# Kernel optimization log

Hardware: AMD Instinct MI355X
Metric: run time of the kernel (lower is better)

The kernel has to match this reference:

```python
import jax, jax.numpy as jnp
import numpy as np

B, S, T = 4, 1024, 2048
HID = 1024
NH = 16
NKV = 4
HD = HID // NH  # 64


def setup_inputs() -> dict:
    key = jax.random.key(0)
    ks = jax.random.split(key, 6)
    scale = 1.0 / np.sqrt(HID)
    return {
        "x": jax.random.normal(ks[0], (B, S, HID), dtype=jnp.float32),
        "context": jax.random.normal(ks[1], (B, T, HID), dtype=jnp.float32),
        "Wq": jax.random.normal(ks[2], (NH * HD, HID), dtype=jnp.float32) * scale,
        "Wk": jax.random.normal(ks[3], (NKV * HD, HID), dtype=jnp.float32) * scale,
        "Wv": jax.random.normal(ks[4], (NKV * HD, HID), dtype=jnp.float32) * scale,
        "Wo": jax.random.normal(ks[5], (HID, NH * HD), dtype=jnp.float32) * scale,
    }


def reference(x, context, Wq, Wk, Wv, Wo):
    Bx, Sx, _ = x.shape
    Tx = context.shape[1]
    rep = NH // NKV
    # projections (Linear with no bias: y = x @ W.T)
    q = (x @ Wq.T).reshape(Bx, Sx, NKV, rep, HD)          # group query heads by KV head
    k = (context @ Wk.T).reshape(Bx, Tx, NKV, HD)
    v = (context @ Wv.T).reshape(Bx, Tx, NKV, HD)
    scale = 1.0 / jnp.sqrt(jnp.asarray(HD, dtype=q.dtype))
    # scores: [B, NKV, rep, S, T] -- shares K across the rep grouped heads
    # (math-identical to repeat_interleave then SDPA, without materializing K/V copies)
    scores = jnp.einsum("bsgrd,btgd->bgrst", q, k) * scale
    attn = jax.nn.softmax(scores, axis=-1)
    out = jnp.einsum("bgrst,btgd->bsgrd", attn, v)        # [B,S,NKV,rep,HD]
    out = out.reshape(Bx, Sx, NH * HD)
    return out @ Wo.T
```

## Files before the change

kernel.cpp:

```cpp
#include <hip/hip_runtime.h>
#include <hip/hip_bf16.h>
#include <stdint.h>

typedef __bf16 bf16x8 __attribute__((ext_vector_type(8)));
typedef float f32x4 __attribute__((ext_vector_type(4)));
typedef unsigned short u16;
typedef unsigned int u32;

struct __align__(8) us4 { u16 x, y, z, w; };
struct __align__(16) us8 { u16 v[8]; };

#define LOG2E 1.44269504088896f
#define QSCALE (0.125f * LOG2E)

__device__ __forceinline__ void async_load16(const void* g, void* l) {
    __builtin_amdgcn_global_load_lds(
        (const __attribute__((address_space(1))) u32*)(uintptr_t)g,
        (__attribute__((address_space(3))) u32*)(u32)(uintptr_t)l,
        16, 0, 0);
}

__device__ __forceinline__ u16 f2bfbits(float f) {
    __bf16 h = (__bf16)f;
    return __builtin_bit_cast(u16, h);
}

__global__ __launch_bounds__(256) void convert_all(
    const float* __restrict__ x, const float* __restrict__ ctx,
    const float* __restrict__ wq, const float* __restrict__ wk,
    const float* __restrict__ wv, const float* __restrict__ wo,
    u16* __restrict__ xb, u16* __restrict__ ctxb, u16* __restrict__ wqb,
    u16* __restrict__ wkb, u16* __restrict__ wvb, u16* __restrict__ wob) {
    int i = blockIdx.x * 256 + threadIdx.x;
    const float* s; u16* d; int j;
    if (i < 524288)        { s = x;   d = xb;   j = i; }
    else if (i < 1572864)  { s = ctx; d = ctxb; j = i - 524288; }
    else if (i < 1703936)  { s = wq;  d = wqb;  j = i - 1572864; }
    else if (i < 1736704)  { s = wk;  d = wkb;  j = i - 1703936; }
    else if (i < 1769472)  { s = wv;  d = wvb;  j = i - 1736704; }
    else                   { s = wo;  d = wob;  j = i - 1769472; }
    const float4* sp = (const float4*)s + (size_t)j * 2;
    float4 a = sp[0], b = sp[1];
    us8 o;
    o.v[0] = f2bfbits(a.x); o.v[1] = f2bfbits(a.y);
    o.v[2] = f2bfbits(a.z); o.v[3] = f2bfbits(a.w);
    o.v[4] = f2bfbits(b.x); o.v[5] = f2bfbits(b.y);
    o.v[6] = f2bfbits(b.z); o.v[7] = f2bfbits(b.w);
    *(us8*)(d + (size_t)j * 8) = o;
}

__global__ __launch_bounds__(256) void proj_qkv(
    const u16* __restrict__ xb, const u16* __restrict__ ctxb,
    const u16* __restrict__ Wqb, const u16* __restrict__ Wkb,
    const u16* __restrict__ Wvb,
    u16* __restrict__ q, u16* __restrict__ k2, u16* __restrict__ vT) {
    __shared__ u16 As[128 * 64];
    __shared__ u16 Bs[128 * 64];
    const int tid = threadIdx.x;
    const int w = tid >> 6, lane = tid & 63, quad = lane >> 4, id = lane & 15;
    const int wr = (w >> 1) * 64, wc = (w & 1) * 64;
    const int lrow = lane >> 3, lcol = (lane & 7) * 8;

    const int bid = blockIdx.x;
    const u16 *A, *Bm;
    int mtile, ntile, mode;
    if (bid < 256) {
        mode = 0; A = xb; Bm = Wqb;
        mtile = (bid >> 3) * 128; ntile = (bid & 7) * 128;
    } else {
        int t = bid - 256, z = t >> 7, r = t & 127;
        mode = 1 + z; A = ctxb; Bm = z ? Wvb : Wkb;
        mtile = (r >> 1) * 128; ntile = (r & 1) * 128;
    }

    f32x4 acc[4][4];
#pragma unroll
    for (int i = 0; i < 4; i++)
#pragma unroll
        for (int j = 0; j < 4; j++) acc[i][j] = (f32x4){0.f, 0.f, 0.f, 0.f};

    for (int k0 = 0; k0 < 1024; k0 += 64) {
        __syncthreads();
#pragma unroll
        for (int is = 0; is < 4; is++) {
            int r = is * 32 + w * 8 + lrow;
            async_load16(A + (size_t)(mtile + r) * 1024 + k0 + lcol, &As[(is * 32 + w * 8) * 64]);
        }
#pragma unroll
        for (int is = 0; is < 4; is++) {
            int r = is * 32 + w * 8 + lrow;
            async_load16(Bm + (size_t)(ntile + r) * 1024 + k0 + lcol, &Bs[(is * 32 + w * 8) * 64]);
        }
        __syncthreads();
#pragma unroll
        for (int kk = 0; kk < 2; kk++) {
            bf16x8 af[4], bfr[4];
#pragma unroll
            for (int i = 0; i < 4; i++)
                af[i] = *(const bf16x8*)&As[(wr + i * 16 + id) * 64 + kk * 32 + quad * 8];
#pragma unroll
            for (int j = 0; j < 4; j++)
                bfr[j] = *(const bf16x8*)&Bs[(wc + j * 16 + id) * 64 + kk * 32 + quad * 8];
#pragma unroll
            for (int i = 0; i < 4; i++)
#pragma unroll
                for (int j = 0; j < 4; j++)
                    acc[i][j] = __builtin_amdgcn_mfma_f32_16x16x32_bf16(af[i], bfr[j], acc[i][j], 0, 0, 0);
        }
    }

#pragma unroll
    for (int i = 0; i < 4; i++)
#pragma unroll
        for (int j = 0; j < 4; j++) {
            int mbase = mtile + wr + i * 16 + quad * 4;
            int n = ntile + wc + j * 16 + id;
            if (mode == 2) {
                int b = mbase >> 11, t = mbase & 2047;
                int g = n >> 6, d = n & 63;
                us4 pk;
                pk.x = f2bfbits(acc[i][j][0]);
                pk.y = f2bfbits(acc[i][j][1]);
                pk.z = f2bfbits(acc[i][j][2]);
                pk.w = f2bfbits(acc[i][j][3]);
                *(us4*)&vT[((size_t)((b << 2) + g) * 64 + d) * 2048 + t] = pk;
            } else if (mode == 1) {
#pragma unroll
                for (int r = 0; r < 4; r++) {
                    int m = mbase + r;
                    int b = m >> 11, t = m & 2047;
                    int g = n >> 6, d = n & 63;
                    k2[((size_t)((b << 2) + g) * 2048 + t) * 64 + d] = f2bfbits(acc[i][j][r]);
                }
            } else {
#pragma unroll
                for (int r = 0; r < 4; r++)
                    q[(size_t)(mbase + r) * 1024 + n] = f2bfbits(acc[i][j][r] * QSCALE);
            }
        }
}

__global__ __launch_bounds__(256) void gemm_out(const u16* __restrict__ A,
                                                const u16* __restrict__ Bm,
                                                float* __restrict__ C) {
    __shared__ u16 As[128 * 64];
    __shared__ u16 Bs[128 * 64];
    const int tid = threadIdx.x;
    const int w = tid >> 6, lane = tid & 63, quad = lane >> 4, id = lane & 15;
    const int mtile = blockIdx.y * 128, ntile = blockIdx.x * 128;
    const int wr = (w >> 1) * 64, wc = (w & 1) * 64;
    const int lrow = lane >> 3, lcol = (lane & 7) * 8;

    f32x4 acc[4][4];
#pragma unroll
    for (int i = 0; i < 4; i++)
#pragma unroll
        for (int j = 0; j < 4; j++) acc[i][j] = (f32x4){0.f, 0.f, 0.f, 0.f};

    for (int k0 = 0; k0 < 1024; k0 += 64) {
        __syncthreads();
#pragma unroll
        for (int is = 0; is < 4; is++) {
            int r = is * 32 + w * 8 + lrow;
            async_load16(A + (size_t)(mtile + r) * 1024 + k0 + lcol, &As[(is * 32 + w * 8) * 64]);
        }
#pragma unroll
        for (int is = 0; is < 4; is++) {
            int r = is * 32 + w * 8 + lrow;
            async_load16(Bm + (size_t)(ntile + r) * 1024 + k0 + lcol, &Bs[(is * 32 + w * 8) * 64]);
        }
        __syncthreads();
#pragma unroll
        for (int kk = 0; kk < 2; kk++) {
            bf16x8 af[4], bfr[4];
#pragma unroll
            for (int i = 0; i < 4; i++)
                af[i] = *(const bf16x8*)&As[(wr + i * 16 + id) * 64 + kk * 32 + quad * 8];
#pragma unroll
            for (int j = 0; j < 4; j++)
                bfr[j] = *(const bf16x8*)&Bs[(wc + j * 16 + id) * 64 + kk * 32 + quad * 8];
#pragma unroll
            for (int i = 0; i < 4; i++)
#pragma unroll
                for (int j = 0; j < 4; j++)
                    acc[i][j] = __builtin_amdgcn_mfma_f32_16x16x32_bf16(af[i], bfr[j], acc[i][j], 0, 0, 0);
        }
    }

#pragma unroll
    for (int i = 0; i < 4; i++)
#pragma unroll
        for (int j = 0; j < 4; j++) {
            int mbase = mtile + wr + i * 16 + quad * 4;
            int n = ntile + wc + j * 16 + id;
#pragma unroll
            for (int r = 0; r < 4; r++)
                C[(size_t)(mbase + r) * 1024 + n] = acc[i][j][r];
        }
}

__global__ __launch_bounds__(256) void attn_kernel(const u16* __restrict__ q,
                                                   const u16* __restrict__ k2,
                                                   const u16* __restrict__ vT,
                                                   u16* __restrict__ o) {
    __shared__ u16 Ks[2][64 * 64];
    __shared__ u16 Vt[2][64 * 64];
    __shared__ u16 Ps[4 * 32 * 72];
    const int tid = threadIdx.x;
    const int w = tid >> 6, lane = tid & 63, quad = lane >> 4, id = lane & 15;

    const int bid = blockIdx.x;
    const int xcd = bid & 7, slot = bid >> 3;
    const int bg = xcd * 2 + (slot >> 5);
    const int inner = slot & 31;
    const int b = bg >> 2, g = bg & 3;
    const int h = g * 4 + (inner >> 3);
    const int s0 = (inner & 7) * 128;

    const int stgswz = (((lane & 7) ^ (lane >> 3)) * 8);
    const int rdsw = id & 7;

    bf16x8 qf[2][2];
#pragma unroll
    for (int rb = 0; rb < 2; rb++) {
        const size_t base = ((size_t)(b * 1024 + s0 + w * 32 + rb * 16 + id)) * 1024 + h * 64;
        qf[rb][0] = *(const bf16x8*)&q[base + quad * 8];
        qf[rb][1] = *(const bf16x8*)&q[base + 32 + quad * 8];
    }

    bf16x8 ones;
    {
        __bf16 one = (__bf16)1.0f;
#pragma unroll
        for (int i = 0; i < 8; i++) ones[i] = one;
    }

    f32x4 acc[2][4], accl[2];
#pragma unroll
    for (int rb = 0; rb < 2; rb++) {
        accl[rb] = (f32x4){0.f, 0.f, 0.f, 0.f};
#pragma unroll
        for (int i = 0; i < 4; i++) acc[rb][i] = (f32x4){0.f, 0.f, 0.f, 0.f};
    }

    const size_t kbase = ((size_t)(b * 4 + g)) * 2048 * 64;
    const size_t vbase = ((size_t)(b * 4 + g)) * 64 * 2048;
    const int pbase = w * 2304;

    auto stage = [&](int t0, int buf) {
#pragma unroll
        for (int is = 0; is < 2; is++) {
            int tl = is * 32 + w * 8;
            async_load16(&k2[kbase + (size_t)(t0 + tl + (lane >> 3)) * 64 + stgswz],
                         &Ks[buf][tl * 64]);
        }
#pragma unroll
        for (int is = 0; is < 2; is++) {
            int dl = is * 32 + w * 8;
            async_load16(&vT[vbase + (size_t)(dl + (lane >> 3)) * 2048 + t0 + stgswz],
                         &Vt[buf][dl * 64]);
        }
    };

    stage(0, 0);
    __syncthreads();

    int cur = 0;
    for (int t0 = 0; t0 < 2048; t0 += 64) {
        if (t0 + 64 < 2048) stage(t0 + 64, cur ^ 1);

        f32x4 s[2][4];
#pragma unroll
        for (int rb = 0; rb < 2; rb++)
#pragma unroll
            for (int cb = 0; cb < 4; cb++) s[rb][cb] = (f32x4){0.f, 0.f, 0.f, 0.f};
#pragma unroll
        for (int kk = 0; kk < 2; kk++)
#pragma unroll
            for (int cb = 0; cb < 4; cb++) {
                bf16x8 kf = *(const bf16x8*)&Ks[cur][(cb * 16 + id) * 64 + (((kk * 4 + quad) ^ rdsw) * 8)];
                s[0][cb] = __builtin_amdgcn_mfma_f32_16x16x32_bf16(qf[0][kk], kf, s[0][cb], 0, 0, 0);
                s[1][cb] = __builtin_amdgcn_mfma_f32_16x16x32_bf16(qf[1][kk], kf, s[1][cb], 0, 0, 0);
            }

#pragma unroll
        for (int rb = 0; rb < 2; rb++)
#pragma unroll
            for (int cb = 0; cb < 4; cb++)
#pragma unroll
                for (int r = 0; r < 4; r++)
                    Ps[pbase + (rb * 16 + quad * 4 + r) * 72 + cb * 16 + id] =
                        f2bfbits(__builtin_exp2f(s[rb][cb][r]));

#pragma unroll
        for (int kk = 0; kk < 2; kk++) {
            bf16x8 pf0 = *(const bf16x8*)&Ps[pbase + id * 72 + kk * 32 + quad * 8];
            bf16x8 pf1 = *(const bf16x8*)&Ps[pbase + (16 + id) * 72 + kk * 32 + quad * 8];
            accl[0] = __builtin_amdgcn_mfma_f32_16x16x32_bf16(pf0, ones, accl[0], 0, 0, 0);
            accl[1] = __builtin_amdgcn_mfma_f32_16x16x32_bf16(pf1, ones, accl[1], 0, 0, 0);
#pragma unroll
            for (int db = 0; db < 4; db++) {
                bf16x8 vf = *(const bf16x8*)&Vt[cur][(db * 16 + id) * 64 + (((kk * 4 + quad) ^ rdsw) * 8)];
                acc[0][db] = __builtin_amdgcn_mfma_f32_16x16x32_bf16(pf0, vf, acc[0][db], 0, 0, 0);
                acc[1][db] = __builtin_amdgcn_mfma_f32_16x16x32_bf16(pf1, vf, acc[1][db], 0, 0, 0);
            }
        }

        __syncthreads();
        cur ^= 1;
    }

#pragma unroll
    for (int rb = 0; rb < 2; rb++) {
        f32x4 inv;
#pragma unroll
        for (int r = 0; r < 4; r++) inv[r] = 1.0f / accl[rb][r];
#pragma unroll
        for (int db = 0; db < 4; db++)
#pragma unroll
            for (int r = 0; r < 4; r++) {
                int srow = s0 + w * 32 + rb * 16 + quad * 4 + r;
                o[((size_t)(b * 1024 + srow)) * 1024 + h * 64 + db * 16 + id] =
                    f2bfbits(acc[rb][db][r] * inv[r]);
            }
    }
}

extern "C" void kernel_launch(void* const* d_in, const int* in_sizes, int n_in,
                              void* d_out, int out_size, void* d_ws, size_t ws_size,
                              hipStream_t stream) {
    (void)in_sizes; (void)n_in; (void)out_size; (void)ws_size;
    const float* x   = (const float*)d_in[0];
    const float* ctx = (const float*)d_in[1];
    const float* Wq  = (const float*)d_in[2];
    const float* Wk  = (const float*)d_in[3];
    const float* Wv  = (const float*)d_in[4];
    const float* Wo  = (const float*)d_in[5];
    float* out = (float*)d_out;

    u16* xb   = (u16*)d_ws;
    u16* ctxb = xb   + 4096 * 1024;
    u16* Wqb  = ctxb + 4 * 2048 * 1024;
    u16* Wkb  = Wqb  + 1024 * 1024;
    u16* Wvb  = Wkb  + 256 * 1024;
    u16* Wob  = Wvb  + 256 * 1024;
    u16* q    = Wob  + 1024 * 1024;
    u16* k2   = q    + 4096 * 1024;
    u16* vT   = k2   + 4 * 4 * 2048 * 64;
    u16* o    = vT   + 4 * 4 * 64 * 2048;

    convert_all<<<7424, 256, 0, stream>>>(x, ctx, Wq, Wk, Wv, Wo,
                                          xb, ctxb, Wqb, Wkb, Wvb, Wob);
    proj_qkv<<<512, 256, 0, stream>>>(xb, ctxb, Wqb, Wkb, Wvb, q, k2, vT);
    attn_kernel<<<512, 256, 0, stream>>>(q, k2, vT, o);
    gemm_out<<<dim3(8, 32), 256, 0, stream>>>(o, Wob, out);
}
```

Baseline: 225.1 us.

## Keep softmax probabilities in registers and shrink GEMM N-tiles to 64

The attention kernel now computes scores transposed (K as the A operand), so each lane's exp2 results already form a bf16x8 P fragment for the PV MFMA. This removes the per-wave LDS round trip for P and needs new K/V swizzle keys so row permutations line up. The projection and output GEMMs move from 128x128 to 128x64 tiles, doubling grid size, and get occupancy launch bounds. The trade-off is more blocks and more redundant A-tile loads in exchange for better CU fill.

After: 205.0 us. -8.9%, faster.

```diff
diff --git a/kernel.cpp b/kernel.cpp
--- a/kernel.cpp
+++ b/kernel.cpp
@@ -49,35 +49,39 @@
     *(us8*)(d + (size_t)j * 8) = o;
 }
 
-__global__ __launch_bounds__(256) void proj_qkv(
+__global__ __launch_bounds__(256, 4) void proj_qkv(
     const u16* __restrict__ xb, const u16* __restrict__ ctxb,
     const u16* __restrict__ Wqb, const u16* __restrict__ Wkb,
     const u16* __restrict__ Wvb,
     u16* __restrict__ q, u16* __restrict__ k2, u16* __restrict__ vT) {
     __shared__ u16 As[128 * 64];
-    __shared__ u16 Bs[128 * 64];
+    __shared__ u16 Bs[64 * 64];
     const int tid = threadIdx.x;
     const int w = tid >> 6, lane = tid & 63, quad = lane >> 4, id = lane & 15;
-    const int wr = (w >> 1) * 64, wc = (w & 1) * 64;
+    const int wr = (w >> 1) * 64, wc = (w & 1) * 32;
     const int lrow = lane >> 3, lcol = (lane & 7) * 8;
 
     const int bid = blockIdx.x;
     const u16 *A, *Bm;
     int mtile, ntile, mode;
-    if (bid < 256) {
+    if (bid < 512) {
         mode = 0; A = xb; Bm = Wqb;
-        mtile = (bid >> 3) * 128; ntile = (bid & 7) * 128;
+        mtile = (bid >> 4) * 128; ntile = (bid & 15) * 64;
+    } else if (bid < 768) {
+        int s2 = bid - 512;
+        mode = 1; A = ctxb; Bm = Wkb;
+        mtile = (s2 >> 2) * 128; ntile = (s2 & 3) * 64;
     } else {
-        int t = bid - 256, z = t >> 7, r = t & 127;
-        mode = 1 + z; A = ctxb; Bm = z ? Wvb : Wkb;
-        mtile = (r >> 1) * 128; ntile = (r & 1) * 128;
-    }
-
-    f32x4 acc[4][4];
+        int s2 = bid - 768;
+        mode = 2; A = ctxb; Bm = Wvb;
+        mtile = (s2 >> 2) * 128; ntile = (s2 & 3) * 64;
+    }
+
+    f32x4 acc[4][2];
 #pragma unroll
     for (int i = 0; i < 4; i++)
 #pragma unroll
-        for (int j = 0; j < 4; j++) acc[i][j] = (f32x4){0.f, 0.f, 0.f, 0.f};
+        for (int j = 0; j < 2; j++) acc[i][j] = (f32x4){0.f, 0.f, 0.f, 0.f};
 
     for (int k0 = 0; k0 < 1024; k0 += 64) {
         __syncthreads();
@@ -87,24 +91,24 @@
             async_load16(A + (size_t)(mtile + r) * 1024 + k0 + lcol, &As[(is * 32 + w * 8) * 64]);
         }
 #pragma unroll
-        for (int is = 0; is < 4; is++) {
+        for (int is = 0; is < 2; is++) {
             int r = is * 32 + w * 8 + lrow;
             async_load16(Bm + (size_t)(ntile + r) * 1024 + k0 + lcol, &Bs[(is * 32 + w * 8) * 64]);
         }
         __syncthreads();
 #pragma unroll
         for (int kk = 0; kk < 2; kk++) {
-            bf16x8 af[4], bfr[4];
+            bf16x8 af[4], bfr[2];
 #pragma unroll
             for (int i = 0; i < 4; i++)
                 af[i] = *(const bf16x8*)&As[(wr + i * 16 + id) * 64 + kk * 32 + quad * 8];
 #pragma unroll
-            for (int j = 0; j < 4; j++)
+            for (int j = 0; j < 2; j++)
                 bfr[j] = *(const bf16x8*)&Bs[(wc + j * 16 + id) * 64 + kk * 32 + quad * 8];
 #pragma unroll
             for (int i = 0; i < 4; i++)
 #pragma unroll
-                for (int j = 0; j < 4; j++)
+                for (int j = 0; j < 2; j++)
                     acc[i][j] = __builtin_amdgcn_mfma_f32_16x16x32_bf16(af[i], bfr[j], acc[i][j], 0, 0, 0);
         }
     }
@@ -112,7 +116,7 @@
 #pragma unroll
     for (int i = 0; i < 4; i++)
 #pragma unroll
-        for (int j = 0; j < 4; j++) {
+        for (int j = 0; j < 2; j++) {
             int mbase = mtile + wr + i * 16 + quad * 4;
             int n = ntile + wc + j * 16 + id;
             if (mode == 2) {
@@ -140,22 +144,22 @@
         }
 }
 
-__global__ __launch_bounds__(256) void gemm_out(const u16* __restrict__ A,
-                                                const u16* __restrict__ Bm,
-                                                float* __restrict__ C) {
+__global__ __launch_bounds__(256, 4) void gemm_out(const u16* __restrict__ A,
+                                                   const u16* __restrict__ Bm,
+                                                   float* __restrict__ C) {
     __shared__ u16 As[128 * 64];
-    __shared__ u16 Bs[128 * 64];
+    __shared__ u16 Bs[64 * 64];
     const int tid = threadIdx.x;
     const int w = tid >> 6, lane = tid & 63, quad = lane >> 4, id = lane & 15;
-    const int mtile = blockIdx.y * 128, ntile = blockIdx.x * 128;
-    const int wr = (w >> 1) * 64, wc = (w & 1) * 64;
+    const int mtile = blockIdx.y * 128, ntile = blockIdx.x * 64;
+    const int wr = (w >> 1) * 64, wc = (w & 1) * 32;
     const int lrow = lane >> 3, lcol = (lane & 7) * 8;
 
-    f32x4 acc[4][4];
+    f32x4 acc[4][2];
 #pragma unroll
     for (int i = 0; i < 4; i++)
 #pragma unroll
-        for (int j = 0; j < 4; j++) acc[i][j] = (f32x4){0.f, 0.f, 0.f, 0.f};
+        for (int j = 0; j < 2; j++) acc[i][j] = (f32x4){0.f, 0.f, 0.f, 0.f};
 
     for (int k0 = 0; k0 < 1024; k0 += 64) {
         __syncthreads();
@@ -165,24 +169,24 @@
             async_load16(A + (size_t)(mtile + r) * 1024 + k0 + lcol, &As[(is * 32 + w * 8) * 64]);
         }
 #pragma unroll
-        for (int is = 0; is < 4; is++) {
+        for (int is = 0; is < 2; is++) {
             int r = is * 32 + w * 8 + lrow;
             async_load16(Bm + (size_t)(ntile + r) * 1024 + k0 + lcol, &Bs[(is * 32 + w * 8) * 64]);
         }
         __syncthreads();
 #pragma unroll
         for (int kk = 0; kk < 2; kk++) {
-            bf16x8 af[4], bfr[4];
+            bf16x8 af[4], bfr[2];
 #pragma unroll
             for (int i = 0; i < 4; i++)
                 af[i] = *(const bf16x8*)&As[(wr + i * 16 + id) * 64 + kk * 32 + quad * 8];
 #pragma unroll
-            for (int j = 0; j < 4; j++)
+            for (int j = 0; j < 2; j++)
                 bfr[j] = *(const bf16x8*)&Bs[(wc + j * 16 + id) * 64 + kk * 32 + quad * 8];
 #pragma unroll
             for (int i = 0; i < 4; i++)
 #pragma unroll
-                for (int j = 0; j < 4; j++)
+                for (int j = 0; j < 2; j++)
                     acc[i][j] = __builtin_amdgcn_mfma_f32_16x16x32_bf16(af[i], bfr[j], acc[i][j], 0, 0, 0);
         }
     }
@@ -190,7 +194,7 @@
 #pragma unroll
     for (int i = 0; i < 4; i++)
 #pragma unroll
-        for (int j = 0; j < 4; j++) {
+        for (int j = 0; j < 2; j++) {
             int mbase = mtile + wr + i * 16 + quad * 4;
             int n = ntile + wc + j * 16 + id;
 #pragma unroll
@@ -199,13 +203,12 @@
         }
 }
 
-__global__ __launch_bounds__(256) void attn_kernel(const u16* __restrict__ q,
-                                                   const u16* __restrict__ k2,
-                                                   const u16* __restrict__ vT,
-                                                   u16* __restrict__ o) {
+__global__ __launch_bounds__(256, 2) void attn_kernel(const u16* __restrict__ q,
+                                                      const u16* __restrict__ k2,
+                                                      const u16* __restrict__ vT,
+                                                      u16* __restrict__ o) {
     __shared__ u16 Ks[2][64 * 64];
     __shared__ u16 Vt[2][64 * 64];
-    __shared__ u16 Ps[4 * 32 * 72];
     const int tid = threadIdx.x;
     const int w = tid >> 6, lane = tid & 63, quad = lane >> 4, id = lane & 15;
 
@@ -217,8 +220,13 @@
     const int h = g * 4 + (inner >> 3);
     const int s0 = (inner & 7) * 128;
 
-    const int stgswz = (((lane & 7) ^ (lane >> 3)) * 8);
-    const int rdsw = id & 7;
+    const int stgswz = (((lane & 7) ^ (lane >> 3) ^ ((w & 1) << 2))) * 8;
+    int kfkey[2];
+#pragma unroll
+    for (int c = 0; c < 2; c++)
+        kfkey[c] = (id & 3) | (((c ^ ((id >> 2) & 1)) & 1) << 2);
+    const int vkey = (id & 7) ^ (((id >> 3) & 1) << 2);
+    const int trow_base = ((id & 12) << 1) + (id & 3);
 
     bf16x8 qf[2][2];
 #pragma unroll
@@ -245,7 +253,6 @@
 
     const size_t kbase = ((size_t)(b * 4 + g)) * 2048 * 64;
     const size_t vbase = ((size_t)(b * 4 + g)) * 64 * 2048;
-    const int pbase = w * 2304;
 
     auto stage = [&](int t0, int buf) {
 #pragma unroll
@@ -269,41 +276,48 @@
     for (int t0 = 0; t0 < 2048; t0 += 64) {
         if (t0 + 64 < 2048) stage(t0 + 64, cur ^ 1);
 
-        f32x4 s[2][4];
+        f32x4 s[2][2][2];
+#pragma unroll
+        for (int kk = 0; kk < 2; kk++)
+#pragma unroll
+            for (int P = 0; P < 2; P++)
+#pragma unroll
+                for (int c = 0; c < 2; c++) {
+                    int trow = P * 32 + trow_base + c * 4;
+                    bf16x8 kf = *(const bf16x8*)&Ks[cur][trow * 64 + (((kk * 4 + quad) ^ kfkey[c]) * 8)];
+#pragma unroll
+                    for (int rb = 0; rb < 2; rb++)
+                        s[rb][P][c] = __builtin_amdgcn_mfma_f32_16x16x32_bf16(
+                            kf, qf[rb][kk],
+                            kk ? s[rb][P][c] : (f32x4){0.f, 0.f, 0.f, 0.f}, 0, 0, 0);
+                }
+
+        bf16x8 pa[2][2];
 #pragma unroll
         for (int rb = 0; rb < 2; rb++)
 #pragma unroll
-            for (int cb = 0; cb < 4; cb++) s[rb][cb] = (f32x4){0.f, 0.f, 0.f, 0.f};
-#pragma unroll
-        for (int kk = 0; kk < 2; kk++)
-#pragma unroll
-            for (int cb = 0; cb < 4; cb++) {
-                bf16x8 kf = *(const bf16x8*)&Ks[cur][(cb * 16 + id) * 64 + (((kk * 4 + quad) ^ rdsw) * 8)];
-                s[0][cb] = __builtin_amdgcn_mfma_f32_16x16x32_bf16(qf[0][kk], kf, s[0][cb], 0, 0, 0);
-                s[1][cb] = __builtin_amdgcn_mfma_f32_16x16x32_bf16(qf[1][kk], kf, s[1][cb], 0, 0, 0);
+            for (int P = 0; P < 2; P++) {
+                bf16x8 t;
+#pragma unroll
+                for (int c = 0; c < 2; c++)
+#pragma unroll
+                    for (int r = 0; r < 4; r++)
+                        t[c * 4 + r] = (__bf16)__builtin_exp2f(s[rb][P][c][r]);
+                pa[rb][P] = t;
             }
 
 #pragma unroll
-        for (int rb = 0; rb < 2; rb++)
-#pragma unroll
-            for (int cb = 0; cb < 4; cb++)
-#pragma unroll
-                for (int r = 0; r < 4; r++)
-                    Ps[pbase + (rb * 16 + quad * 4 + r) * 72 + cb * 16 + id] =
-                        f2bfbits(__builtin_exp2f(s[rb][cb][r]));
-
-#pragma unroll
-        for (int kk = 0; kk < 2; kk++) {
-            bf16x8 pf0 = *(const bf16x8*)&Ps[pbase + id * 72 + kk * 32 + quad * 8];
-            bf16x8 pf1 = *(const bf16x8*)&Ps[pbase + (16 + id) * 72 + kk * 32 + quad * 8];
-            accl[0] = __builtin_amdgcn_mfma_f32_16x16x32_bf16(pf0, ones, accl[0], 0, 0, 0);
-            accl[1] = __builtin_amdgcn_mfma_f32_16x16x32_bf16(pf1, ones, accl[1], 0, 0, 0);
+        for (int P = 0; P < 2; P++) {
 #pragma unroll
             for (int db = 0; db < 4; db++) {
-                bf16x8 vf = *(const bf16x8*)&Vt[cur][(db * 16 + id) * 64 + (((kk * 4 + quad) ^ rdsw) * 8)];
-                acc[0][db] = __builtin_amdgcn_mfma_f32_16x16x32_bf16(pf0, vf, acc[0][db], 0, 0, 0);
-                acc[1][db] = __builtin_amdgcn_mfma_f32_16x16x32_bf16(pf1, vf, acc[1][db], 0, 0, 0);
+                bf16x8 vf = *(const bf16x8*)&Vt[cur][(db * 16 + id) * 64 + (((P * 4 + quad) ^ vkey) * 8)];
+#pragma unroll
+                for (int rb = 0; rb < 2; rb++)
+                    acc[rb][db] = __builtin_amdgcn_mfma_f32_16x16x32_bf16(pa[rb][P], vf, acc[rb][db], 0, 0, 0);
             }
+#pragma unroll
+            for (int rb = 0; rb < 2; rb++)
+                accl[rb] = __builtin_amdgcn_mfma_f32_16x16x32_bf16(pa[rb][P], ones, accl[rb], 0, 0, 0);
         }
 
         __syncthreads();
@@ -351,7 +365,7 @@
 
     convert_all<<<7424, 256, 0, stream>>>(x, ctx, Wq, Wk, Wv, Wo,
                                           xb, ctxb, Wqb, Wkb, Wvb, Wob);
-    proj_qkv<<<512, 256, 0, stream>>>(xb, ctxb, Wqb, Wkb, Wvb, q, k2, vT);
+    proj_qkv<<<1024, 256, 0, stream>>>(xb, ctxb, Wqb, Wkb, Wvb, q, k2, vT);
     attn_kernel<<<512, 256, 0, stream>>>(q, k2, vT, o);
-    gemm_out<<<dim3(8, 32), 256, 0, stream>>>(o, Wob, out);
-}
+    gemm_out<<<dim3(16, 32), 256, 0, stream>>>(o, Wob, out);
+}
```
